# Performance work log

Measured on AMD Instinct MI355X. Metric: run time of the kernel, lower is better.

The kernel has to match this reference:

```python
import jax, jax.numpy as jnp
import numpy as np

S, B, W, H = 97, 256, 1024, 16
HD = W // H


def setup_inputs() -> dict:
    key = jax.random.key(0)
    ks = jax.random.split(key, 16)
    def p(k, shape):
        return jax.random.normal(k, shape, jnp.float32) * 0.02
    return {
        "tensor": jax.random.normal(ks[0], (S, B, W), jnp.float32),
        "mask": jnp.zeros((S, S), jnp.float32),
        "q_w": p(ks[1], (W, W)), "q_b": p(ks[2], (W,)),
        "k_w": p(ks[3], (W, W)), "k_b": p(ks[4], (W,)),
        "v_w": p(ks[5], (W, W)), "v_b": p(ks[6], (W,)),
        "in_proj_w": p(ks[7], (3 * W, W)), "in_proj_b": p(ks[8], (3 * W,)),
        "mha_out_w": p(ks[9], (W, W)), "mha_out_b": p(ks[10], (W,)),
        "out_w": p(ks[11], (W, W)), "out_b": p(ks[12], (W,)),
    }


def _freqs_cos_sin(dim, seqlen, theta=10000.0):
    # matches precompute_freqs_cis: angle[t, j] = t / theta**(2j/dim)
    inv = 1.0 / (theta ** (jnp.arange(0, dim, 2, dtype=jnp.float32) / dim))  # (dim/2,)
    ang = jnp.arange(seqlen, dtype=jnp.float32)[:, None] * inv[None, :]      # (S, dim/2)
    return jnp.cos(ang)[:, None, :], jnp.sin(ang)[:, None, :]                # (S, 1, dim/2)


def _rotary(x, cos, sin):
    # x: (S, B, D); pairs (even, odd) along last dim form complex numbers
    s, b, d = x.shape
    xr = x.reshape(s, b, d // 2, 2)
    xe, xo = xr[..., 0], xr[..., 1]
    oe = xe * cos - xo * sin
    oo = xe * sin + xo * cos
    return jnp.stack([oe, oo], axis=-1).reshape(s, b, d)


def reference(tensor, mask, q_w, q_b, k_w, k_b, v_w, v_b,
              in_proj_w, in_proj_b, mha_out_w, mha_out_b, out_w, out_b):
    # tensor: (S, B, W) -- torch MHA default batch_first=False layout
    q = tensor @ q_w.T + q_b
    k = tensor @ k_w.T + k_b
    v = tensor @ v_w.T + v_b

    cos, sin = _freqs_cos_sin(W, S)
    q = _rotary(q, cos, sin)
    k = _rotary(k, cos, sin)

    # nn.MultiheadAttention internal in_proj (applied on top of q/k/v linears)
    Wq, Wk, Wv = in_proj_w[:W], in_proj_w[W:2 * W], in_proj_w[2 * W:]
    bq, bk, bv = in_proj_b[:W], in_proj_b[W:2 * W], in_proj_b[2 * W:]
    q = q @ Wq.T + bq
    k = k @ Wk.T + bk
    v = v @ Wv.T + bv

    def split_heads(x):  # (S,B,W) -> (B,H,S,HD)
        return x.reshape(S, B, H, HD).transpose(1, 2, 0, 3)

    qh, kh, vh = split_heads(q), split_heads(k), split_heads(v)
    scale = 1.0 / jnp.sqrt(jnp.float32(HD))
    scores = jnp.einsum('bhqd,bhkd->bhqk', qh, kh) * scale + mask  # additive float mask
    attn = jax.nn.softmax(scores, axis=-1)
    o = jnp.einsum('bhqk,bhkd->bhqd', attn, vh)      # (B,H,S,HD)
    o = o.transpose(2, 0, 1, 3).reshape(S, B, W)     # (S,B,W)
    o = o @ mha_out_w.T + mha_out_b                  # MHA out_proj
    return o @ out_w.T + out_b                       # module's final self.out
```

## Files before the change

### kernel.cpp

```cpp
#include <hip/hip_runtime.h>
#include <cstdint>
#include <cstddef>

#define S_LEN 97
#define B_DIM 256
#define W_DIM 1024
#define NH    16
#define HDIM  64
#define MROWS (S_LEN * B_DIM)

typedef unsigned short u16;
typedef __bf16 bf16x8 __attribute__((ext_vector_type(8)));
typedef float  f32x4  __attribute__((ext_vector_type(4)));

__device__ __forceinline__ u16 f2bf(float f) {
  __bf16 b = (__bf16)f;
  return __builtin_bit_cast(unsigned short, b);
}
__device__ __forceinline__ float bf2f(u16 h) {
  union { uint32_t u; float f; } v; v.u = ((uint32_t)h) << 16;
  return v.f;
}

__device__ __forceinline__ void gload16(const void* g, void* lds) {
  __builtin_amdgcn_global_load_lds(
      (const __attribute__((address_space(1))) void*)(uintptr_t)g,
      (__attribute__((address_space(3))) void*)(uint32_t)(uintptr_t)lds,
      16, 0, 0);
}

__global__ void k_cvt(const float* __restrict__ s, u16* __restrict__ d, int n4) {
  int i = blockIdx.x * blockDim.x + threadIdx.x;
  if (i >= n4) return;
  float4 v = ((const float4*)s)[i];
  uint2 pk;
  pk.x = (uint32_t)f2bf(v.x) | ((uint32_t)f2bf(v.y) << 16);
  pk.y = (uint32_t)f2bf(v.z) | ((uint32_t)f2bf(v.w) << 16);
  ((uint2*)d)[i] = pk;
}

__global__ void k_cvt_t(const float* __restrict__ src, u16* __restrict__ dst) {
  __shared__ float t[32][33];
  const int bx = blockIdx.x * 32, by = blockIdx.y * 32;
  const int tx = threadIdx.x, ty = threadIdx.y;
  for (int yy = ty; yy < 32; yy += 8)
    t[yy][tx] = src[(size_t)(by + yy) * 1024 + bx + tx];
  __syncthreads();
  for (int yy = ty; yy < 32; yy += 8)
    dst[(size_t)(bx + yy) * 1024 + by + tx] = f2bf(t[tx][yy]);
}

__global__ void k_bias2(const float* a, const float* b, float* dst) {
  int i = blockIdx.x * blockDim.x + threadIdx.x;
  if (i >= 2 * W_DIM) return;
  dst[i] = (i < W_DIM) ? a[i] : b[i - W_DIM];
}

__global__ void k_zero(float* dst, int n) {
  int i = blockIdx.x * blockDim.x + threadIdx.x;
  if (i < n) dst[i] = 0.f;
}

__global__ void k_maskpad(const float* __restrict__ mask, float* __restrict__ mp) {
  int i = blockIdx.x * blockDim.x + threadIdx.x;
  int r = i >> 7, c = i & 127;
  float v;
  if (c >= S_LEN) v = -1e30f;
  else if (r < S_LEN) v = mask[r * S_LEN + c];
  else v = 0.f;
  mp[i] = v;
}

__global__ void k_biasfold(const float* __restrict__ M, const float* __restrict__ v,
                           const float* __restrict__ b2, float* __restrict__ out) {
  const int lane = threadIdx.x & 63, wave = threadIdx.x >> 6;
  const int row = blockIdx.x * 4 + wave;
  float s = 0.f;
  for (int k = lane; k < 1024; k += 64) s += M[(size_t)row * 1024 + k] * v[k];
#pragma unroll
  for (int d = 32; d; d >>= 1) s += __shfl_xor(s, d);
  if (lane == 0) out[row] = s + b2[row];
}

__global__ void k_rope_tab(float* __restrict__ tab) {
  int idx = blockIdx.x * blockDim.x + threadIdx.x;
  if (idx >= S_LEN * 512) return;
  int s = idx / 512, i = idx % 512;
  float freq = expf(-(float)i * (9.210340371976184f / 512.0f));
  float ang = (float)s * freq;
  float sv, cv;
  sincosf(ang, &sv, &cv);
  tab[idx * 2 + 0] = cv;
  tab[idx * 2 + 1] = sv;
}

template <int OUT_MODE>
__global__ __launch_bounds__(256) void k_gemm(
    const u16* __restrict__ A, int lda, const u16* __restrict__ Bw,
    const float* __restrict__ bias, void* __restrict__ Cp, int ldc, int K) {
  __shared__ u16 As[128 * 64];
  __shared__ u16 Bs[128 * 64];

  const int tid = threadIdx.x, lane = tid & 63, wave = tid >> 6;
  const int wm = wave >> 1, wn = wave & 1;
  const int m0 = blockIdx.y * 128;
  const int n0 = blockIdx.x * 128;

  f32x4 acc[4][4] = {};

  const int lrow = lane >> 3;
  const int lcol = (lane & 7) * 8;
  const u16* Ag = A + (size_t)(m0 + wave * 8 + lrow) * lda + lcol;
  const u16* Bg = Bw + (size_t)(n0 + wave * 8 + lrow) * K + lcol;
  u16* Asl = As + wave * 8 * 64;
  u16* Bsl = Bs + wave * 8 * 64;

  for (int kt = 0; kt < K; kt += 64) {
#pragma unroll
    for (int i = 0; i < 4; ++i) {
      gload16(Ag + (size_t)(i * 32) * lda + kt, Asl + i * 2048);
      gload16(Bg + (size_t)(i * 32) * K + kt, Bsl + i * 2048);
    }
    __syncthreads();
#pragma unroll
    for (int kk = 0; kk < 2; ++kk) {
      bf16x8 af[4], bfr[4];
#pragma unroll
      for (int m = 0; m < 4; ++m)
        af[m] = *(const bf16x8*)(As + (wm * 64 + m * 16 + (lane & 15)) * 64 + kk * 32 + (lane >> 4) * 8);
#pragma unroll
      for (int n = 0; n < 4; ++n)
        bfr[n] = *(const bf16x8*)(Bs + (wn * 64 + n * 16 + (lane & 15)) * 64 + kk * 32 + (lane >> 4) * 8);
#pragma unroll
      for (int m = 0; m < 4; ++m)
#pragma unroll
        for (int n = 0; n < 4; ++n)
          acc[m][n] = __builtin_amdgcn_mfma_f32_16x16x32_bf16(af[m], bfr[n], acc[m][n], 0, 0, 0);
    }
    __syncthreads();
  }

  const int r0 = (lane >> 4) * 4;
  const int c0 = lane & 15;
#pragma unroll
  for (int m = 0; m < 4; ++m) {
#pragma unroll
    for (int n = 0; n < 4; ++n) {
      const int col = n0 + wn * 64 + n * 16 + c0;
      const float bv = bias[col];
#pragma unroll
      for (int r = 0; r < 4; ++r) {
        const int row = m0 + wm * 64 + m * 16 + r0 + r;
        const float v = acc[m][n][r] + bv;
        if (OUT_MODE == 0) {
          ((u16*)Cp)[(size_t)row * ldc + col] = f2bf(v);
        } else if (OUT_MODE == 2) {
          ((float*)Cp)[(size_t)row * ldc + col] = v;
        }
      }
    }
  }
}

template <int OUT_MODE, int ACOLB, int SCALEQ = 0>
__global__ __launch_bounds__(512, 2) void k_gemm256(
    const u16* __restrict__ A, int lda, const u16* __restrict__ Bw,
    const float* __restrict__ bias, void* __restrict__ Cp, int ldc,
    size_t thirdStride, const float* __restrict__ tab, int Nt) {
  __shared__ u16 lds[2 * 32768];

  const int tid = threadIdx.x, lane = tid & 63, wave = tid >> 6;
  const int wm = wave >> 2, wn = wave & 3;
  const int c0 = lane & 15, hi = lane >> 4;

  const int nwg = gridDim.x;
  const int qq = nwg >> 3, rr_ = nwg & 7;
  const int xcd = blockIdx.x & 7, sub = blockIdx.x >> 3;
  const int seq = (xcd < rr_ ? xcd * (qq + 1) : rr_ * (qq + 1) + (xcd - rr_) * qq) + sub;
  const int mt = seq / Nt, nt = seq - mt * Nt;
  const int m0 = mt * 256, n0 = nt * 256;
  const int aoff = ACOLB ? (n0 & ~1023) : 0;

  const int rl = tid >> 3, pc = tid & 7;
  const int gc = pc ^ (rl & 7);
  const u16* aS = A + (size_t)(m0 + rl) * lda + aoff + gc * 8;
  const u16* bS = Bw + (size_t)(n0 + rl) * 1024 + gc * 8;
  const uint32_t ldsW = wave * 512;

  auto stageR = [&](int tt, int L) {
    const int bb = (tt & 1) * 32768;
    const u16* src = (L < 4) ? (aS + (size_t)(L * 64) * lda + tt * 64)
                             : (bS + (size_t)((L - 4) * 64) * 1024 + tt * 64);
    gload16(src, (u16*)lds + bb + L * 4096 + ldsW);
  };

  int aofr[2][8], bofr[2][4];
#pragma unroll
  for (int kk = 0; kk < 2; ++kk) {
#pragma unroll
    for (int m = 0; m < 8; ++m)
      aofr[kk][m] = (wm * 128 + m * 16 + c0) * 64 + (((kk * 4 + hi) ^ (c0 & 7)) * 8);
#pragma unroll
    for (int n = 0; n < 4; ++n)
      bofr[kk][n] = 16384 + (wn * 64 + n * 16 + c0) * 64 + (((kk * 4 + hi) ^ (c0 & 7)) * 8);
  }

  stageR(0, 0); stageR(0, 1); stageR(0, 2); stageR(0, 3);
  stageR(0, 4); stageR(0, 5); stageR(0, 6); stageR(0, 7);
  asm volatile("s_waitcnt vmcnt(0)" ::: "memory");
  __builtin_amdgcn_s_barrier();

  f32x4 acc[8][4] = {};
  bf16x8 afP[4], afN[4], bfrC[4], bfrN[4];

  {
    const u16* buf = lds;
#pragma unroll
    for (int n = 0; n < 4; ++n) bfrC[n] = *(const bf16x8*)(buf + bofr[0][n]);
#pragma unroll
    for (int m = 0; m < 4; ++m) afP[m] = *(const bf16x8*)(buf + aofr[0][m]);
  }

#define MFMA16(MB, AF, BF)                                                      \
  _Pragma("unroll") for (int m = 0; m < 4; ++m)                                 \
  _Pragma("unroll") for (int n = 0; n < 4; ++n)                                 \
      acc[(MB) + m][n] =                                                        \
          __builtin_amdgcn_mfma_f32_16x16x32_bf16(AF[m], BF[n], acc[(MB) + m][n], 0, 0, 0);

  for (int t = 0; t < 16; ++t) {
    const u16* buf = lds + (t & 1) * 32768;
    const u16* nbuf = lds + ((t + 1) & 1) * 32768;
    const bool pf = (t < 15);

#pragma unroll
    for (int m = 0; m < 4; ++m) afN[m] = *(const bf16x8*)(buf + aofr[0][4 + m]);
    if (pf) { stageR(t + 1, 0); stageR(t + 1, 2); stageR(t + 1, 4); }
    __builtin_amdgcn_s_setprio(1);
    MFMA16(0, afP, bfrC);
    __builtin_amdgcn_s_setprio(0);

#pragma unroll
    for (int n = 0; n < 4; ++n) bfrN[n] = *(const bf16x8*)(buf + bofr[1][n]);
#pragma unroll
    for (int m = 0; m < 4; ++m) afP[m] = *(const bf16x8*)(buf + aofr[1][m]);
    if (pf) { stageR(t + 1, 5); stageR(t + 1, 6); stageR(t + 1, 7); }
    __builtin_amdgcn_s_setprio(1);
    MFMA16(4, afN, bfrC);
    __builtin_amdgcn_s_setprio(0);

#pragma unroll
    for (int m = 0; m < 4; ++m) afN[m] = *(const bf16x8*)(buf + aofr[1][4 + m]);
    if (pf) { stageR(t + 1, 1); stageR(t + 1, 3); }
    __builtin_amdgcn_s_setprio(1);
    MFMA16(0, afP, bfrN);
    __builtin_amdgcn_s_setprio(0);

    __builtin_amdgcn_s_setprio(1);
    MFMA16(4, afN, bfrN);
    __builtin_amdgcn_s_setprio(0);

    if (pf) {
      asm volatile("s_waitcnt vmcnt(0)" ::: "memory");
      __builtin_amdgcn_s_barrier();
#pragma unroll
      for (int n = 0; n < 4; ++n) bfrC[n] = *(const bf16x8*)(nbuf + bofr[0][n]);
#pragma unroll
      for (int m = 0; m < 4; ++m) afP[m] = *(const bf16x8*)(nbuf + aofr[0][m]);
    }
  }
#undef MFMA16

  const int r0 = (lane >> 4) * 4;
#pragma unroll
  for (int m = 0; m < 8; ++m) {
#pragma unroll
    for (int n = 0; n < 4; ++n) {
      const int col = n0 + wn * 64 + n * 16 + c0;
      const float bv = bias[col];
      if (OUT_MODE == 3) {
        const int pairI = (col & 1023) >> 1;
        const float sgn = (col & 1) ? 1.f : -1.f;
#pragma unroll
        for (int r = 0; r < 4; ++r) {
          const int row = m0 + wm * 128 + m * 16 + r0 + r;
          const float v = acc[m][n][r] + bv;
          const float p = __shfl_xor(v, 1);
          const float2 cs = ((const float2*)tab)[(row >> 8) * 512 + pairI];
          ((u16*)Cp)[(size_t)row * ldc + col] = f2bf(v * cs.x + sgn * p * cs.y);
        }
      } else {
#pragma unroll
        for (int r = 0; r < 4; ++r) {
          const int row = m0 + wm * 128 + m * 16 + r0 + r;
          const float v = acc[m][n][r] + bv;
          if (OUT_MODE == 0) {
            ((u16*)Cp)[(size_t)row * ldc + col] = f2bf(v);
          } else if (OUT_MODE == 2) {
            ((float*)Cp)[(size_t)row * ldc + col] = v;
          } else {
            const int which = col >> 10, c = col & 1023;
            const int h = c >> 6, d = c & 63;
            const int s = row >> 8, b = row & 255;
            const float sc = (SCALEQ && which == 0) ? 0.125f : 1.0f;
            ((u16*)Cp)[(size_t)which * thirdStride +
                       (((size_t)(b * NH + h) * S_LEN + s) * HDIM + d)] = f2bf(v * sc);
          }
        }
      }
    }
  }
}

__global__ __launch_bounds__(512, 4) void k_attn(const u16* __restrict__ qkv2,
                                                 const float* __restrict__ maskP,
                                                 u16* __restrict__ O1) {
  __shared__ u16 Vt[80 * 128];
  __shared__ u16 Pb[128 * 128];
  __shared__ float redS[128];

  const size_t TS = (size_t)MROWS * W_DIM;
  const int bh = blockIdx.x, b = bh >> 4, h = bh & 15;
  const int tid = threadIdx.x, lane = tid & 63, wave = tid >> 6;
  const int wm = wave >> 2;
  const int wn = wave & 3;
  const int c0 = lane & 15, hi = lane >> 4;

  const u16* Qg = qkv2 + (size_t)bh * (S_LEN * HDIM);
  const u16* Kg = Qg + TS;
  const u16* Vg = Qg + 2 * TS;

  float mk[4][2][4];
#pragma unroll
  for (int m = 0; m < 4; ++m)
#pragma unroll
    for (int n = 0; n < 2; ++n)
#pragma unroll
      for (int r = 0; r < 4; ++r)
        mk[m][n][r] = maskP[(wm * 64 + m * 16 + hi * 4 + r) * 128 + wn * 32 + n * 16 + c0];

  for (int idx = tid; idx < 1024; idx += 512) {
    const int s = idx >> 3, c = (idx & 7) * 8;
    uint4 vv = make_uint4(0, 0, 0, 0);
    if (s < S_LEN) vv = *(const uint4*)(Vg + (size_t)s * HDIM + c);
    u16 tmp[8];
    *(uint4*)tmp = vv;
#pragma unroll
    for (int j = 0; j < 8; ++j)
      Vt[(c + j) * 128 + (s ^ (j << 3))] = tmp[j];
  }
  if (tid < 128) Vt[64 * 128 + tid] = 0x3F80;

  f32x4 acc[4][2] = {};
#pragma unroll
  for (int kk = 0; kk < 2; ++kk) {
    bf16x8 af[4], bfr[2];
#pragma unroll
    for (int m = 0; m < 4; ++m)
      af[m] = *(const bf16x8*)(Qg + (size_t)(wm * 64 + m * 16 + c0) * HDIM + kk * 32 + hi * 8);
#pragma unroll
    for (int n = 0; n < 2; ++n)
      bfr[n] = *(const bf16x8*)(Kg + (size_t)(wn * 32 + n * 16 + c0) * HDIM + kk * 32 + hi * 8);
#pragma unroll
    for (int m = 0; m < 4; ++m)
#pragma unroll
      for (int n = 0; n < 2; ++n)
        acc[m][n] = __builtin_amdgcn_mfma_f32_16x16x32_bf16(af[m], bfr[n], acc[m][n], 0, 0, 0);
  }

#pragma unroll
  for (int m = 0; m < 4; ++m) {
#pragma unroll
    for (int r = 0; r < 4; ++r) {
      const int row = wm * 64 + m * 16 + hi * 4 + r;
#pragma unroll
      for (int n = 0; n < 2; ++n) {
        const int col = wn * 32 + n * 16 + c0;
        const float e = __expf(acc[m][n][r] + mk[m][n][r]);
        Pb[row * 128 + (col ^ ((row & 7) << 3))] = f2bf(e);
      }
    }
  }
  __syncthreads();

  f32x4 o[4] = {};
  f32x4 osum[4] = {};
#pragma unroll
  for (int kk = 0; kk < 4; ++kk) {
    bf16x8 pa[4], vb, vbs;
#pragma unroll
    for (int m = 0; m < 4; ++m) {
      const int row = wm * 64 + m * 16 + c0;
      pa[m] = *(const bf16x8*)(Pb + row * 128 + ((kk * 32 + hi * 8) ^ ((row & 7) << 3)));
    }
    {
      const int d = wn * 16 + c0;
      vb = *(const bf16x8*)(Vt + d * 128 + ((kk * 32 + hi * 8) ^ ((d & 7) << 3)));
    }
    if (wn == 0) {
      const int ds = 64 + c0;
      vbs = *(const bf16x8*)(Vt + ds * 128 + ((kk * 32 + hi * 8) ^ ((ds & 7) << 3)));
    }
#pragma unroll
    for (int m = 0; m < 4; ++m)
      o[m] = __builtin_amdgcn_mfma_f32_16x16x32_bf16(pa[m], vb, o[m], 0, 0, 0);
    if (wn == 0) {
#pragma unroll
      for (int m = 0; m < 4; ++m)
        osum[m] = __builtin_amdgcn_mfma_f32_16x16x32_bf16(pa[m], vbs, osum[m], 0, 0, 0);
    }
  }

  if (wn == 0 && c0 == 0) {
#pragma unroll
    for (int m = 0; m < 4; ++m)
#pragma unroll
      for (int r = 0; r < 4; ++r)
        redS[wm * 64 + m * 16 + hi * 4 + r] = osum[m][r];
  }
  __syncthreads();

  u16* Ob = Pb;
#pragma unroll
  for (int m = 0; m < 4; ++m)
#pragma unroll
    for (int r = 0; r < 4; ++r) {
      const int row = wm * 64 + m * 16 + hi * 4 + r;
      const float iv = 1.0f / redS[row];
      Ob[row * 80 + wn * 16 + c0] = f2bf(o[m][r] * iv);
    }
  __syncthreads();

  if (tid < 4 * S_LEN) {
    const int row = tid >> 2, q = tid & 3;
    const u16* src = Ob + row * 80 + q * 16;
    uint4 a0 = *(const uint4*)(src);
    uint4 a1 = *(const uint4*)(src + 8);
    u16* dst = O1 + ((size_t)row * B_DIM + b) * W_DIM + h * HDIM + q * 16;
    *(uint4*)dst = a0;
    *(uint4*)(dst + 8) = a1;
  }
}

extern "C" void kernel_launch(void* const* d_in, const int* in_sizes, int n_in,
                              void* d_out, int out_size, void* d_ws, size_t ws_size,
                              hipStream_t stream) {
  (void)in_sizes; (void)n_in; (void)out_size; (void)ws_size;
  const float* tensor    = (const float*)d_in[0];
  const float* mask      = (const float*)d_in[1];
  const float* q_w       = (const float*)d_in[2];
  const float* q_b       = (const float*)d_in[3];
  const float* k_w       = (const float*)d_in[4];
  const float* k_b       = (const float*)d_in[5];
  const float* v_w       = (const float*)d_in[6];
  const float* v_b       = (const float*)d_in[7];
  const float* in_proj_w = (const float*)d_in[8];
  const float* in_proj_b = (const float*)d_in[9];
  const float* mha_w     = (const float*)d_in[10];
  const float* mha_b     = (const float*)d_in[11];
  const float* out_w     = (const float*)d_in[12];
  const float* out_b     = (const float*)d_in[13];

  char* ws = (char*)d_ws;
  size_t off = 0;
  auto alloc = [&](size_t bytes) {
    char* p = ws + off;
    off += (bytes + 255) & ~(size_t)255;
    return p;
  };

  const size_t TS = (size_t)MROWS * W_DIM;

  float* tab = (float*)alloc((size_t)S_LEN * 512 * 2 * sizeof(float));
  float* maskP = (float*)alloc((size_t)128 * 128 * sizeof(float));
  u16* Xbf   = (u16*)alloc(TS * 2);
  u16* qkv1  = (u16*)alloc((size_t)MROWS * 2048 * 2);
  u16* qkv2  = (u16*)alloc(TS * 3 * 2);
  u16* WC1   = (u16*)alloc((size_t)2048 * 1024 * 2);
  u16* W2    = (u16*)alloc((size_t)3072 * 1024 * 2);
  u16* WvT   = (u16*)alloc((size_t)1024 * 1024 * 2);
  u16* WmT   = (u16*)alloc((size_t)1024 * 1024 * 2);
  u16* WO    = (u16*)alloc((size_t)1024 * 1024 * 2);
  u16* WVf   = (u16*)alloc((size_t)1024 * 1024 * 2);
  u16* WFf   = (u16*)alloc((size_t)1024 * 1024 * 2);
  float* bc1 = (float*)alloc(2048 * sizeof(float));
  float* bvf = (float*)alloc(1024 * sizeof(float));
  float* bff = (float*)alloc(1024 * sizeof(float));
  float* zb  = (float*)alloc(1024 * sizeof(float));
  u16* O1 = Xbf;

  k_rope_tab<<<dim3((S_LEN * 512 + 255) / 256), 256, 0, stream>>>(tab);
  k_maskpad<<<dim3(64), 256, 0, stream>>>(mask, maskP);
  k_cvt<<<dim3(MROWS * W_DIM / 4 / 256), 256, 0, stream>>>(tensor, Xbf, MROWS * W_DIM / 4);
  k_cvt<<<dim3(1024), 256, 0, stream>>>(q_w, WC1, 262144);
  k_cvt<<<dim3(1024), 256, 0, stream>>>(k_w, WC1 + 1048576, 262144);
  k_cvt<<<dim3(3072), 256, 0, stream>>>(in_proj_w, W2, 786432);
  k_cvt<<<dim3(1024), 256, 0, stream>>>(out_w, WO, 262144);
  k_cvt_t<<<dim3(32, 32), dim3(32, 8), 0, stream>>>(v_w, WvT);
  k_cvt_t<<<dim3(32, 32), dim3(32, 8), 0, stream>>>(mha_w, WmT);
  k_bias2<<<dim3(8), 256, 0, stream>>>(q_b, k_b, bc1);
  k_zero<<<dim3(4), 256, 0, stream>>>(zb, 1024);
  k_biasfold<<<dim3(256), 256, 0, stream>>>(in_proj_w + (size_t)2048 * 1024, v_b,
                                            in_proj_b + 2048, bvf);
  k_biasfold<<<dim3(256), 256, 0, stream>>>(out_w, mha_b, out_b, bff);

  k_gemm<0><<<dim3(8, 8), 256, 0, stream>>>(
      W2 + (size_t)2048 * 1024, 1024, WvT, zb, WVf, 1024, 1024);
  k_gemm<0><<<dim3(8, 8), 256, 0, stream>>>(
      WO, 1024, WmT, zb, WFf, 1024, 1024);

  k_gemm256<3, 0><<<dim3(97 * 8), 512, 0, stream>>>(
      Xbf, W_DIM, WC1, bc1, qkv1, 2048, 0, tab, 8);

  k_gemm256<1, 0><<<dim3(97 * 4), 512, 0, stream>>>(
      Xbf, W_DIM, WVf, bvf, qkv2 + 2 * TS, 0, TS, nullptr, 4);

  k_gemm256<1, 1, 1><<<dim3(97 * 8), 512, 0, stream>>>(
      qkv1, 2048, W2, in_proj_b, qkv2, 0, TS, nullptr, 8);

  k_attn<<<dim3(B_DIM * NH), 512, 0, stream>>>(qkv2, maskP, O1);

  k_gemm256<2, 0><<<dim3(97 * 4), 512, 0, stream>>>(
      O1, W_DIM, WFf, bff, d_out, W_DIM, 0, nullptr, 4);
}
```

Baseline: 579.3 us.

## Switch 256-tile GEMM to triple-buffered K=32 LDS pipeline with prefetch depth two

The 256x256 GEMM kernel now uses three 16K-element LDS slots with a K step of 32 instead of two 32K slots with a K step of 64. Loads are issued two iterations ahead, and the wait is vmcnt(4) rather than a full drain, so global loads stay in flight across barriers. LDS use drops from 128 KB to 96 KB. The cost is twice as many barriers and iterations, and new LDS offset math with wave-to-K-half assignment that could be wrong.

After: 585.6 us. About the same (+1.1%).

```diff
diff --git a/kernel.cpp b/kernel.cpp
--- a/kernel.cpp
+++ b/kernel.cpp
@@ -167,7 +167,7 @@
     const u16* __restrict__ A, int lda, const u16* __restrict__ Bw,
     const float* __restrict__ bias, void* __restrict__ Cp, int ldc,
     size_t thirdStride, const float* __restrict__ tab, int Nt) {
-  __shared__ u16 lds[2 * 32768];
+  __shared__ u16 lds[3 * 16384];
 
   const int tid = threadIdx.x, lane = tid & 63, wave = tid >> 6;
   const int wm = wave >> 2, wn = wave & 3;
@@ -181,45 +181,51 @@
   const int m0 = mt * 256, n0 = nt * 256;
   const int aoff = ACOLB ? (n0 & ~1023) : 0;
 
-  const int rl = tid >> 3, pc = tid & 7;
-  const int gc = pc ^ (rl & 7);
-  const u16* aS = A + (size_t)(m0 + rl) * lda + aoff + gc * 8;
-  const u16* bS = Bw + (size_t)(n0 + rl) * 1024 + gc * 8;
-  const uint32_t ldsW = wave * 512;
-
-  auto stageR = [&](int tt, int L) {
-    const int bb = (tt & 1) * 32768;
-    const u16* src = (L < 4) ? (aS + (size_t)(L * 64) * lda + tt * 64)
-                             : (bS + (size_t)((L - 4) * 64) * 1024 + tt * 64);
-    gload16(src, (u16*)lds + bb + L * 4096 + ldsW);
+  const int Lb = tid >> 3, pc = tid & 7;
+  const int lcl = pc ^ (Lb & 7);
+  const int rsel = lcl >> 2;
+  const int csel = (lcl & 3) * 8;
+  const u16* aSrc[2]; const u16* bSrc[2];
+  uint32_t dOff[2];
+#pragma unroll
+  for (int rh = 0; rh < 2; ++rh) {
+    const int row = 64 * rh + Lb + 128 * rsel;
+    aSrc[rh] = A + (size_t)(m0 + row) * lda + aoff + csel;
+    bSrc[rh] = Bw + (size_t)(n0 + row) * 1024 + csel;
+    dOff[rh] = rh * 4096 + wave * 512;
+  }
+  auto stageA = [&](int tt, int rh, u16* slot) {
+    gload16(aSrc[rh] + tt * 32, slot + dOff[rh]);
   };
-
-  int aofr[2][8], bofr[2][4];
-#pragma unroll
-  for (int kk = 0; kk < 2; ++kk) {
-#pragma unroll
-    for (int m = 0; m < 8; ++m)
-      aofr[kk][m] = (wm * 128 + m * 16 + c0) * 64 + (((kk * 4 + hi) ^ (c0 & 7)) * 8);
-#pragma unroll
-    for (int n = 0; n < 4; ++n)
-      bofr[kk][n] = 16384 + (wn * 64 + n * 16 + c0) * 64 + (((kk * 4 + hi) ^ (c0 & 7)) * 8);
-  }
-
-  stageR(0, 0); stageR(0, 1); stageR(0, 2); stageR(0, 3);
-  stageR(0, 4); stageR(0, 5); stageR(0, 6); stageR(0, 7);
-  asm volatile("s_waitcnt vmcnt(0)" ::: "memory");
+  auto stageB = [&](int tt, int rh, u16* slot) {
+    gload16(bSrc[rh] + tt * 32, slot + 8192 + dOff[rh]);
+  };
+
+  int aofr[8], bofr[4];
+#pragma unroll
+  for (int m = 0; m < 8; ++m)
+    aofr[m] = (m * 16 + c0) * 64 + ((((wm << 2) | hi) ^ (c0 & 7)) * 8);
+#pragma unroll
+  for (int n = 0; n < 4; ++n)
+    bofr[n] = 8192 + ((wn & 1) * 64 + n * 16 + c0) * 64 +
+              (((((wn >> 1) << 2) | hi) ^ (c0 & 7)) * 8);
+
+  u16* s0 = lds;
+  u16* s1 = lds + 16384;
+  u16* s2 = lds + 32768;
+
+  stageA(0, 0, s0); stageA(0, 1, s0); stageB(0, 0, s0); stageB(0, 1, s0);
+  stageA(1, 0, s1); stageA(1, 1, s1); stageB(1, 0, s1); stageB(1, 1, s1);
+  asm volatile("s_waitcnt vmcnt(4)" ::: "memory");
   __builtin_amdgcn_s_barrier();
+  __builtin_amdgcn_sched_barrier(0);
 
   f32x4 acc[8][4] = {};
-  bf16x8 afP[4], afN[4], bfrC[4], bfrN[4];
-
-  {
-    const u16* buf = lds;
-#pragma unroll
-    for (int n = 0; n < 4; ++n) bfrC[n] = *(const bf16x8*)(buf + bofr[0][n]);
-#pragma unroll
-    for (int m = 0; m < 4; ++m) afP[m] = *(const bf16x8*)(buf + aofr[0][m]);
-  }
+  bf16x8 afP[4], afN[4], bfrC[4];
+#pragma unroll
+  for (int n = 0; n < 4; ++n) bfrC[n] = *(const bf16x8*)(s0 + bofr[n]);
+#pragma unroll
+  for (int m = 0; m < 4; ++m) afP[m] = *(const bf16x8*)(s0 + aofr[m]);
 
 #define MFMA16(MB, AF, BF)                                                      \
   _Pragma("unroll") for (int m = 0; m < 4; ++m)                                 \
@@ -227,45 +233,31 @@
       acc[(MB) + m][n] =                                                        \
           __builtin_amdgcn_mfma_f32_16x16x32_bf16(AF[m], BF[n], acc[(MB) + m][n], 0, 0, 0);
 
-  for (int t = 0; t < 16; ++t) {
-    const u16* buf = lds + (t & 1) * 32768;
-    const u16* nbuf = lds + ((t + 1) & 1) * 32768;
-    const bool pf = (t < 15);
-
-#pragma unroll
-    for (int m = 0; m < 4; ++m) afN[m] = *(const bf16x8*)(buf + aofr[0][4 + m]);
-    if (pf) { stageR(t + 1, 0); stageR(t + 1, 2); stageR(t + 1, 4); }
+  for (int t = 0; t < 32; ++t) {
+    const bool pf = (t < 30);
+
+#pragma unroll
+    for (int m = 0; m < 4; ++m) afN[m] = *(const bf16x8*)(s0 + aofr[4 + m]);
+    if (pf) { stageA(t + 2, 0, s2); stageA(t + 2, 1, s2); }
     __builtin_amdgcn_s_setprio(1);
     MFMA16(0, afP, bfrC);
     __builtin_amdgcn_s_setprio(0);
 
-#pragma unroll
-    for (int n = 0; n < 4; ++n) bfrN[n] = *(const bf16x8*)(buf + bofr[1][n]);
-#pragma unroll
-    for (int m = 0; m < 4; ++m) afP[m] = *(const bf16x8*)(buf + aofr[1][m]);
-    if (pf) { stageR(t + 1, 5); stageR(t + 1, 6); stageR(t + 1, 7); }
+    if (pf) { stageB(t + 2, 0, s2); stageB(t + 2, 1, s2); }
     __builtin_amdgcn_s_setprio(1);
     MFMA16(4, afN, bfrC);
     __builtin_amdgcn_s_setprio(0);
 
-#pragma unroll
-    for (int m = 0; m < 4; ++m) afN[m] = *(const bf16x8*)(buf + aofr[1][4 + m]);
-    if (pf) { stageR(t + 1, 1); stageR(t + 1, 3); }
-    __builtin_amdgcn_s_setprio(1);
-    MFMA16(0, afP, bfrN);
-    __builtin_amdgcn_s_setprio(0);
-
-    __builtin_amdgcn_s_setprio(1);
-    MFMA16(4, afN, bfrN);
-    __builtin_amdgcn_s_setprio(0);
-
-    if (pf) {
-      asm volatile("s_waitcnt vmcnt(0)" ::: "memory");
+    if (t < 31) {
+      if (t < 30) asm volatile("s_waitcnt vmcnt(4)" ::: "memory");
+      else        asm volatile("s_waitcnt vmcnt(0)" ::: "memory");
       __builtin_amdgcn_s_barrier();
-#pragma unroll
-      for (int n = 0; n < 4; ++n) bfrC[n] = *(const bf16x8*)(nbuf + bofr[0][n]);
-#pragma unroll
-      for (int m = 0; m < 4; ++m) afP[m] = *(const bf16x8*)(nbuf + aofr[0][m]);
+      __builtin_amdgcn_sched_barrier(0);
+      u16* tmp = s0; s0 = s1; s1 = s2; s2 = tmp;
+#pragma unroll
+      for (int n = 0; n < 4; ++n) bfrC[n] = *(const bf16x8*)(s0 + bofr[n]);
+#pragma unroll
+      for (int m = 0; m < 4; ++m) afP[m] = *(const bf16x8*)(s0 + aofr[m]);
     }
   }
 #undef MFMA16
```
